# Kernel optimization log

Measured on AMD Instinct MI355X. Metric: run time of the kernel, lower is better.

## Reference

```python
import jax, jax.numpy as jnp
import numpy as np

B, S, D, H, L, V, DF = 2, 1024, 1024, 16, 4, 32000, 4096


def setup_inputs() -> dict:
    key = jax.random.key(0)
    ks = iter(jax.random.split(key, 64))
    rn = lambda shape, s=0.02: jax.random.normal(next(ks), shape, jnp.float32) * s
    inp = {
        'dec_input': rn((B, S, D), 1.0),
        'enc_input': rn((B, S, D), 1.0),
        # additive masks: causal for self-attn, none for cross-attn
        'masked_attention_mask': jnp.where(jnp.tril(jnp.ones((S, S), bool)), 0.0, -1e9)[None, None].astype(jnp.float32),
        'cross_attention_mask': jnp.zeros((1, 1, S, S), jnp.float32),
        'num_heads': H,
    }
    for p in ['sWq', 'sWk', 'sWv', 'sWo', 'cWq', 'cWk', 'cWv', 'cWo']:
        inp[p] = rn((L, D, D))
    for p in ['sbq', 'sbk', 'sbv', 'sbo', 'cbq', 'cbk', 'cbv', 'cbo']:
        inp[p] = jnp.zeros((L, D), jnp.float32)
    for p in ['ln1_g', 'ln2_g', 'ln3_g']:
        inp[p] = jnp.ones((L, D), jnp.float32)
    for p in ['ln1_b', 'ln2_b', 'ln3_b']:
        inp[p] = jnp.zeros((L, D), jnp.float32)
    inp['fW1'] = rn((L, D, DF)); inp['fb1'] = jnp.zeros((L, DF), jnp.float32)
    inp['fW2'] = rn((L, DF, D)); inp['fb2'] = jnp.zeros((L, D), jnp.float32)
    inp['Wout'] = rn((D, V)); inp['bout'] = jnp.zeros((V,), jnp.float32)
    return inp


def positional_encoding(seq_len, d_model, n=10000.0):
    # vectorized equivalent of the original triple-nested loop:
    # even d -> sin(i / n^(d/D)); odd d -> cos(i / n^((d-1)/D)); d==0 denom 1 == n^0
    i = jnp.arange(seq_len, dtype=jnp.float32)[:, None]
    d = jnp.arange(d_model)
    denom = jnp.power(n, (2 * (d // 2)).astype(jnp.float32) / d_model)
    ang = i / denom
    return jnp.where(d % 2 == 0, jnp.sin(ang), jnp.cos(ang))  # [S, D]


def layer_norm(x, g, b, eps=1e-5):
    m = jnp.mean(x, -1, keepdims=True)
    v = jnp.mean(jnp.square(x - m), -1, keepdims=True)
    return (x - m) * jax.lax.rsqrt(v + eps) * g + b


def mha(q_in, k_in, v_in, mask, Wq, bq, Wk, bk, Wv, bv, Wo, bo, h):
    b, sq, d = q_in.shape
    dh = d // h
    q = (q_in @ Wq + bq).reshape(b, sq, h, dh)
    k = (k_in @ Wk + bk).reshape(b, -1, h, dh)
    v = (v_in @ Wv + bv).reshape(b, -1, h, dh)
    scores = jnp.einsum('bqhd,bkhd->bhqk', q, k) / jnp.sqrt(jnp.float32(dh)) + mask
    attn = jax.nn.softmax(scores, axis=-1)
    out = jnp.einsum('bhqk,bkhd->bqhd', attn, v).reshape(b, sq, d)
    return out @ Wo + bo


def reference(dec_input, enc_input, masked_attention_mask, cross_attention_mask,
              sWq, sbq, sWk, sbk, sWv, sbv, sWo, sbo,
              cWq, cbq, cWk, cbk, cWv, cbv, cWo, cbo,
              ln1_g, ln1_b, ln2_g, ln2_b, ln3_g, ln3_b,
              fW1, fb1, fW2, fb2, Wout, bout, num_heads):
    b, s, d = dec_input.shape
    x0 = dec_input + positional_encoding(s, d)
    n_layers = sWq.shape[0]
    y = x0
    for l in range(n_layers):
        # NOTE: original DecoderSequential bug: every block consumes the ORIGINAL input;
        # only the last block's output survives.
        a1 = layer_norm(x0 + mha(x0, x0, x0, masked_attention_mask,
                                 sWq[l], sbq[l], sWk[l], sbk[l], sWv[l], sbv[l], sWo[l], sbo[l], num_heads),
                        ln1_g[l], ln1_b[l])
        a2 = layer_norm(a1 + mha(a1, enc_input, enc_input, cross_attention_mask,
                                 cWq[l], cbq[l], cWk[l], cbk[l], cWv[l], cbv[l], cWo[l], cbo[l], num_heads),
                        ln2_g[l], ln2_b[l])
        ff = jax.nn.relu(a2 @ fW1[l] + fb1[l]) @ fW2[l] + fb2[l]
        y = layer_norm(a2 + ff, ln3_g[l], ln3_b[l])
    return y @ Wout + bout  # [B, S, V]
```

## Files before the change

kernel.cpp:

```cpp
#include <hip/hip_runtime.h>
#include <cstdint>
#include <cstddef>

#define DEV __device__ __forceinline__

typedef __attribute__((ext_vector_type(8))) short short8;
typedef __attribute__((ext_vector_type(4))) float f32x4;
typedef __attribute__((ext_vector_type(16))) float f32x16;
typedef __attribute__((ext_vector_type(4))) unsigned short ushort4v;

DEV unsigned short f2bf(float f){
  union { float f; unsigned int i; } v; v.f = f;
  unsigned int r = v.i + 0x7fffu + ((v.i >> 16) & 1u);
  return (unsigned short)(r >> 16);
}

DEV void gld_lds16(const unsigned short* g, unsigned short* lds){
  __builtin_amdgcn_global_load_lds((const __attribute__((address_space(1))) void*)g,
                                   (__attribute__((address_space(3))) void*)lds, 16, 0, 0);
}

DEV int swz(int r, int s){
  int ln = r >> 1;
  int sl = ((r & 1) << 2) | s;
  return ln * 64 + (((sl ^ (ln & 7))) << 3);
}

template<int BN, int EPI>
__global__ __launch_bounds__(256, 2)
void gemm32(const unsigned short* __restrict__ A,
            const unsigned short* __restrict__ Bt,
            const float* __restrict__ bias,
            void* __restrict__ C, int M, int N, int K)
{
  constexpr int NFR  = BN / 64;
  constexpr int ROWS = 128 + BN;
  constexpr int BUFH = ROWS * 32;
  constexpr int GLD  = ROWS / 64;
  __shared__ __align__(16) unsigned short lds[3 * BUFH];

  const int tid = threadIdx.x, wid = tid >> 6, l = tid & 63;
  const int wr = wid >> 1, wcn = wid & 1;

  const int nbm = M / 128, nbn = N / BN;
  const int nwg = nbm * nbn;
  const int q8 = nwg >> 3, r8 = nwg & 7;
  const int xcd = blockIdx.x & 7, within = blockIdx.x >> 3;
  const int wg = (xcd < r8 ? xcd * (q8 + 1) : r8 * (q8 + 1) + (xcd - r8) * q8) + within;
  const int mb = (wg % nbm) * 128, nb = (wg / nbm) * BN;

  const int nk = K / 32;

  const int sL   = tid >> 3;
  const int sSl  = (tid & 7) ^ (sL & 7);
  const int sRow = sL * 2 + (sSl >> 2);
  const int sKc  = (sSl & 3) * 8;

  const int r31 = l & 31, hi = l >> 5;

  int aoff[2][2], boff[NFR][2];
  #pragma unroll
  for (int m = 0; m < 2; m++)
    #pragma unroll
    for (int ks = 0; ks < 2; ks++)
      aoff[m][ks] = wr * 2048 + swz(m * 32 + r31, 2 * ks + hi);
  #pragma unroll
  for (int n = 0; n < NFR; n++){
    const int col = wcn * (BN / 2) + n * 32 + r31;
    #pragma unroll
    for (int ks = 0; ks < 2; ks++)
      boff[n][ks] = 4096 + (col >> 6) * 2048 + swz(col & 63, 2 * ks + hi);
  }

  f32x16 acc[2][NFR];
  #pragma unroll
  for (int m = 0; m < 2; m++)
    #pragma unroll
    for (int n = 0; n < NFR; n++)
      #pragma unroll
      for (int e = 0; e < 16; e++) acc[m][n][e] = 0.f;

#define STAGE_A(c, tt, b2) \
  gld_lds16(A + (size_t)(mb + (c)*64 + sRow) * K + (size_t)(tt)*32 + sKc, \
            lds + (b2)*BUFH + (c)*2048 + tid*8)
#define STAGE_B(c, tt, b2) \
  gld_lds16(Bt + (size_t)(nb + (c)*64 + sRow) * K + (size_t)(tt)*32 + sKc, \
            lds + (b2)*BUFH + 4096 + (c)*2048 + tid*8)
#define WAIT_GLD() do { if constexpr (GLD == 6) asm volatile("s_waitcnt vmcnt(6)" ::: "memory"); \
                        else if constexpr (GLD == 4) asm volatile("s_waitcnt vmcnt(4)" ::: "memory"); \
                        else asm volatile("s_waitcnt vmcnt(3)" ::: "memory"); } while(0)

  STAGE_A(0, 0, 0); STAGE_A(1, 0, 0);
  #pragma unroll
  for (int c = 0; c < NFR; c++) STAGE_B(c, 0, 0);
  if (nk > 1){
    STAGE_A(0, 1, 1); STAGE_A(1, 1, 1);
    #pragma unroll
    for (int c = 0; c < NFR; c++) STAGE_B(c, 1, 1);
    WAIT_GLD();
  } else {
    asm volatile("s_waitcnt vmcnt(0)" ::: "memory");
  }
  asm volatile("" ::: "memory");
  __builtin_amdgcn_s_barrier();
  asm volatile("" ::: "memory");

  int bb = 0;
  for (int u = 0; u < nk; u++){
    const unsigned short* buf = lds + bb * BUFH;
    const int sb = (bb >= 1) ? bb - 1 : 2;
    const bool st = (u + 2 < nk);
    short8 af[2], bf[NFR];

    af[0] = *(const short8*)(buf + aoff[0][0]);
    af[1] = *(const short8*)(buf + aoff[1][0]);
    #pragma unroll
    for (int n = 0; n < NFR; n++) bf[n] = *(const short8*)(buf + boff[n][0]);
    if (st){
      STAGE_A(0, u + 2, sb); STAGE_A(1, u + 2, sb);
      if constexpr (NFR == 4) STAGE_B(0, u + 2, sb);
    }
    __builtin_amdgcn_s_setprio(1);
    #pragma unroll
    for (int m = 0; m < 2; m++)
      #pragma unroll
      for (int n = 0; n < NFR; n++)
        acc[m][n] = __builtin_amdgcn_mfma_f32_32x32x16_bf16(af[m], bf[n], acc[m][n], 0, 0, 0);
    __builtin_amdgcn_s_setprio(0);

    af[0] = *(const short8*)(buf + aoff[0][1]);
    af[1] = *(const short8*)(buf + aoff[1][1]);
    #pragma unroll
    for (int n = 0; n < NFR; n++) bf[n] = *(const short8*)(buf + boff[n][1]);
    if (st){
      if constexpr (NFR == 4){ STAGE_B(1, u + 2, sb); STAGE_B(2, u + 2, sb); STAGE_B(3, u + 2, sb); }
      else if constexpr (NFR == 2){ STAGE_B(0, u + 2, sb); STAGE_B(1, u + 2, sb); }
      else { STAGE_B(0, u + 2, sb); }
    }
    __builtin_amdgcn_s_setprio(1);
    #pragma unroll
    for (int m = 0; m < 2; m++)
      #pragma unroll
      for (int n = 0; n < NFR; n++)
        acc[m][n] = __builtin_amdgcn_mfma_f32_32x32x16_bf16(af[m], bf[n], acc[m][n], 0, 0, 0);
    __builtin_amdgcn_s_setprio(0);

    if (st)               WAIT_GLD();
    else if (u + 1 < nk)  asm volatile("s_waitcnt vmcnt(0)" ::: "memory");
    asm volatile("" ::: "memory");
    __builtin_amdgcn_s_barrier();
    asm volatile("" ::: "memory");
    bb = (bb == 2) ? 0 : bb + 1;
  }
#undef WAIT_GLD
#undef STAGE_A
#undef STAGE_B

  #pragma unroll
  for (int n = 0; n < NFR; n++){
    const int col = nb + wcn * (BN / 2) + n * 32 + r31;
    const float bv = bias ? bias[col] : 0.f;
    #pragma unroll
    for (int m = 0; m < 2; m++){
      const int rowb = mb + wr * 64 + m * 32 + 4 * hi;
      #pragma unroll
      for (int reg = 0; reg < 16; reg++){
        const int row = rowb + (reg & 3) + 8 * (reg >> 2);
        float v = acc[m][n][reg] + bv;
        size_t idx = (size_t)row * N + col;
        if (EPI == 0)       ((float*)C)[idx] = v;
        else if (EPI == 3)  __builtin_nontemporal_store(v, &((float*)C)[idx]);
        else if (EPI == 1)  ((unsigned short*)C)[idx] = f2bf(v);
        else { v = v > 0.f ? v : 0.f; ((unsigned short*)C)[idx] = f2bf(v); }
      }
    }
  }
}

template<int CAUSAL>
__global__ __launch_bounds__(256)
void attn_kernel(const unsigned short* __restrict__ Qb, int ldq,
                 const unsigned short* __restrict__ Kb, int ldk,
                 const unsigned short* __restrict__ Vb, int ldv,
                 unsigned short* __restrict__ Ob, int ldo)
{
  constexpr int S = 1024;
  __shared__ __align__(16) unsigned short vt[64][40];
  __shared__ __align__(16) unsigned short plds[4][16][40];
  const int tid = threadIdx.x, w = tid >> 6, l = tid & 63;
  const int qt = blockIdx.x, bh = blockIdx.y;
  const int b = bh >> 4, h = bh & 15;
  const int hoff = h * 64;
  const size_t rb = (size_t)b * S;

  const int qrow = qt * 64 + w * 16 + (l & 15);
  const unsigned short* qp = Qb + (rb + qrow) * ldq + hoff + ((l >> 4) * 8);
  short8 qf0 = *(const short8*)qp;
  short8 qf1 = *(const short8*)(qp + 32);

  float m_run[4] = {-1e30f, -1e30f, -1e30f, -1e30f};
  float l_run[4] = {0.f, 0.f, 0.f, 0.f};
  f32x4 oacc[4];
  #pragma unroll
  for (int t = 0; t < 4; t++) oacc[t] = (f32x4){0.f, 0.f, 0.f, 0.f};

  const int qmax = qt * 64 + w * 16 + 15;
  const int nkeys = CAUSAL ? (qt * 64 + 64) : S;
  const int skey = tid >> 3, sd8 = (tid & 7) * 8;

  for (int kb = 0; kb < nkeys; kb += 32){
    short8 vv = *(const short8*)(Vb + (rb + kb + skey) * ldv + hoff + sd8);
    #pragma unroll
    for (int i = 0; i < 8; i++) vt[sd8 + i][skey] = (unsigned short)vv[i];
    __syncthreads();
    if (!CAUSAL || kb <= qmax){
      f32x4 sc[2];
      #pragma unroll
      for (int g = 0; g < 2; g++){
        const unsigned short* kp = Kb + (rb + kb + g * 16 + (l & 15)) * ldk + hoff + ((l >> 4) * 8);
        short8 kf0 = *(const short8*)kp;
        short8 kf1 = *(const short8*)(kp + 32);
        f32x4 z = (f32x4){0.f, 0.f, 0.f, 0.f};
        z = __builtin_amdgcn_mfma_f32_16x16x32_bf16(qf0, kf0, z, 0, 0, 0);
        z = __builtin_amdgcn_mfma_f32_16x16x32_bf16(qf1, kf1, z, 0, 0, 0);
        sc[g] = z;
      }
      #pragma unroll
      for (int jj = 0; jj < 4; jj++){
        float s0 = sc[0][jj] * 0.125f, s1 = sc[1][jj] * 0.125f;
        if (CAUSAL){
          int q = qt * 64 + w * 16 + ((l >> 4) << 2) + jj;
          if (kb + (l & 15) > q)      s0 = -1e30f;
          if (kb + 16 + (l & 15) > q) s1 = -1e30f;
        }
        float mx = fmaxf(s0, s1);
        mx = fmaxf(mx, __shfl_xor(mx, 1));
        mx = fmaxf(mx, __shfl_xor(mx, 2));
        mx = fmaxf(mx, __shfl_xor(mx, 4));
        mx = fmaxf(mx, __shfl_xor(mx, 8));
        float mnew = fmaxf(m_run[jj], mx);
        float scal = __expf(m_run[jj] - mnew);
        m_run[jj] = mnew;
        float p0 = __expf(s0 - mnew), p1 = __expf(s1 - mnew);
        float rs = p0 + p1;
        rs += __shfl_xor(rs, 1); rs += __shfl_xor(rs, 2);
        rs += __shfl_xor(rs, 4); rs += __shfl_xor(rs, 8);
        l_run[jj] = l_run[jj] * scal + rs;
        #pragma unroll
        for (int t = 0; t < 4; t++) oacc[t][jj] *= scal;
        int qr = ((l >> 4) << 2) + jj;
        plds[w][qr][l & 15]      = f2bf(p0);
        plds[w][qr][16 + (l & 15)] = f2bf(p1);
      }
      asm volatile("s_waitcnt lgkmcnt(0)" ::: "memory");
      short8 pf = *(const short8*)&plds[w][l & 15][(l >> 4) * 8];
      #pragma unroll
      for (int t = 0; t < 4; t++){
        short8 vf = *(const short8*)&vt[t * 16 + (l & 15)][(l >> 4) * 8];
        oacc[t] = __builtin_amdgcn_mfma_f32_16x16x32_bf16(pf, vf, oacc[t], 0, 0, 0);
      }
    }
    __syncthreads();
  }
  #pragma unroll
  for (int jj = 0; jj < 4; jj++){
    float inv = 1.f / l_run[jj];
    int q = qt * 64 + w * 16 + ((l >> 4) << 2) + jj;
    #pragma unroll
    for (int t = 0; t < 4; t++)
      Ob[(rb + q) * ldo + hoff + t * 16 + (l & 15)] = f2bf(oacc[t][jj] * inv);
  }
}

__global__ __launch_bounds__(256)
void ln_kernel(const float* __restrict__ x1, const float* __restrict__ x2,
               const float* __restrict__ g, const float* __restrict__ be,
               float* __restrict__ outf, unsigned short* __restrict__ outb)
{
  const int row = blockIdx.x, t = threadIdx.x;
  __shared__ float red[4];
  const float4 v1 = ((const float4*)(x1 + (size_t)row * 1024))[t];
  const float4 v2 = ((const float4*)(x2 + (size_t)row * 1024))[t];
  float x[4] = {v1.x + v2.x, v1.y + v2.y, v1.z + v2.z, v1.w + v2.w};
  float s = x[0] + x[1] + x[2] + x[3];
  for (int o = 1; o < 64; o <<= 1) s += __shfl_xor(s, o);
  const int w = t >> 6, l = t & 63;
  if (l == 0) red[w] = s;
  __syncthreads();
  const float mean = (red[0] + red[1] + red[2] + red[3]) * (1.f / 1024.f);
  float d[4]; float sq = 0.f;
  #pragma unroll
  for (int i = 0; i < 4; i++){ d[i] = x[i] - mean; sq += d[i] * d[i]; }
  __syncthreads();
  for (int o = 1; o < 64; o <<= 1) sq += __shfl_xor(sq, o);
  if (l == 0) red[w] = sq;
  __syncthreads();
  const float var = (red[0] + red[1] + red[2] + red[3]) * (1.f / 1024.f);
  const float inv = rsqrtf(var + 1e-5f);
  const int base = t * 4;
  #pragma unroll
  for (int i = 0; i < 4; i++){
    float o = d[i] * inv * g[base + i] + be[base + i];
    if (outf) outf[(size_t)row * 1024 + base + i] = o;
    outb[(size_t)row * 1024 + base + i] = f2bf(o);
  }
}

__global__ __launch_bounds__(256)
void build_x0(const float* __restrict__ dec, float* __restrict__ xf, unsigned short* __restrict__ xb)
{
  const int i = blockIdx.x * 256 + threadIdx.x;
  const int i4 = i * 4;
  const int d0 = i4 & 1023;
  const int s  = (i4 >> 10) & 1023;
  float4 dv = ((const float4*)dec)[i];
  const float* dvp = (const float*)&dv;
  float o[4];
  #pragma unroll
  for (int j = 0; j < 4; j++){
    int dd = d0 + j;
    float e = (float)(dd & ~1) * (1.f / 1024.f);
    float den = expf(e * 9.210340371976184f);
    float ang = (float)s / den;
    float pe = (dd & 1) ? cosf(ang) : sinf(ang);
    o[j] = dvp[j] + pe;
  }
  ((float4*)xf)[i] = make_float4(o[0], o[1], o[2], o[3]);
  ushort4v ob; ob[0] = f2bf(o[0]); ob[1] = f2bf(o[1]); ob[2] = f2bf(o[2]); ob[3] = f2bf(o[3]);
  ((ushort4v*)xb)[i] = ob;
}

__global__ __launch_bounds__(256)
void cvt_bf16_k(const float* __restrict__ in, unsigned short* __restrict__ out)
{
  const int i = blockIdx.x * 256 + threadIdx.x;
  float4 v = ((const float4*)in)[i];
  ushort4v o; o[0] = f2bf(v.x); o[1] = f2bf(v.y); o[2] = f2bf(v.z); o[3] = f2bf(v.w);
  ((ushort4v*)out)[i] = o;
}

__global__ __launch_bounds__(256)
void transpose_cvt(const float* __restrict__ in, unsigned short* __restrict__ out, int R, int C)
{
  __shared__ float t[32][65];
  const int cb = blockIdx.x * 32, rb = blockIdx.y * 64;
  const int tx = threadIdx.x & 31, ty = threadIdx.x >> 5;
  #pragma unroll
  for (int i = 0; i < 8; i++)
    t[tx][ty + 8 * i] = in[(size_t)(rb + ty + 8 * i) * C + cb + tx];
  __syncthreads();
  const int lane = threadIdx.x & 63, cr = threadIdx.x >> 6;
  #pragma unroll
  for (int j = 0; j < 8; j++){
    int c = cr + 4 * j;
    out[(size_t)(cb + c) * R + rb + lane] = f2bf(t[c][lane]);
  }
}

struct TPtrs { const float* src[8]; unsigned short* dst[8]; };
__global__ __launch_bounds__(256)
void transpose_cvt8(TPtrs p)
{
  __shared__ float t[32][65];
  const float* __restrict__ in = p.src[blockIdx.z];
  unsigned short* __restrict__ out = p.dst[blockIdx.z];
  const int cb = blockIdx.x * 32, rb = blockIdx.y * 64;
  const int tx = threadIdx.x & 31, ty = threadIdx.x >> 5;
  #pragma unroll
  for (int i = 0; i < 8; i++)
    t[tx][ty + 8 * i] = in[(size_t)(rb + ty + 8 * i) * 1024 + cb + tx];
  __syncthreads();
  const int lane = threadIdx.x & 63, cr = threadIdx.x >> 6;
  #pragma unroll
  for (int j = 0; j < 8; j++){
    int c = cr + 4 * j;
    out[(size_t)(cb + c) * 1024 + rb + lane] = f2bf(t[c][lane]);
  }
}

__global__ __launch_bounds__(256)
void copy_biases(const float* sbq, const float* sbk, const float* sbv,
                 const float* cbk, const float* cbv,
                 float* bqkv, float* bkvc)
{
  const int i = blockIdx.x * 256 + threadIdx.x;
  const int seg = i >> 10, off = i & 1023;
  if (seg == 0)      bqkv[off] = sbq[off];
  else if (seg == 1) bqkv[1024 + off] = sbk[off];
  else if (seg == 2) bqkv[2048 + off] = sbv[off];
  else if (seg == 3) bkvc[off] = cbk[off];
  else               bkvc[1024 + off] = cbv[off];
}

extern "C" void kernel_launch(void* const* d_in, const int* in_sizes, int n_in,
                              void* d_out, int out_size, void* d_ws, size_t ws_size,
                              hipStream_t stream)
{
  constexpr int S = 1024, D = 1024, V = 32000, DF = 4096;
  constexpr int M = 2 * S;
  constexpr int DD = D * D;
  constexpr int l3 = 3;

  const float* dec  = (const float*)d_in[0];
  const float* enc  = (const float*)d_in[1];
  const float* sWq = (const float*)d_in[5]  + l3 * DD;
  const float* sWk = (const float*)d_in[6]  + l3 * DD;
  const float* sWv = (const float*)d_in[7]  + l3 * DD;
  const float* sWo = (const float*)d_in[8]  + l3 * DD;
  const float* cWq = (const float*)d_in[9]  + l3 * DD;
  const float* cWk = (const float*)d_in[10] + l3 * DD;
  const float* cWv = (const float*)d_in[11] + l3 * DD;
  const float* cWo = (const float*)d_in[12] + l3 * DD;
  const float* sbq = (const float*)d_in[13] + l3 * D;
  const float* sbk = (const float*)d_in[14] + l3 * D;
  const float* sbv = (const float*)d_in[15] + l3 * D;
  const float* sbo = (const float*)d_in[16] + l3 * D;
  const float* cbq = (const float*)d_in[17] + l3 * D;
  const float* cbk = (const float*)d_in[18] + l3 * D;
  const float* cbv = (const float*)d_in[19] + l3 * D;
  const float* cbo = (const float*)d_in[20] + l3 * D;
  const float* ln1g = (const float*)d_in[21] + l3 * D;
  const float* ln2g = (const float*)d_in[22] + l3 * D;
  const float* ln3g = (const float*)d_in[23] + l3 * D;
  const float* ln1b = (const float*)d_in[24] + l3 * D;
  const float* ln2b = (const float*)d_in[25] + l3 * D;
  const float* ln3b = (const float*)d_in[26] + l3 * D;
  const float* fW1 = (const float*)d_in[27] + (size_t)l3 * D * DF;
  const float* fb1 = (const float*)d_in[28] + l3 * DF;
  const float* fW2 = (const float*)d_in[29] + (size_t)l3 * DF * D;
  const float* fb2 = (const float*)d_in[30] + l3 * D;
  const float* Wout = (const float*)d_in[31];
  const float* bout = (const float*)d_in[32];
  float* out = (float*)d_out;

  uint8_t* wsp = (uint8_t*)d_ws;
  auto alloc = [&](size_t bytes) -> void* {
    void* p = wsp; wsp += (bytes + 255) & ~(size_t)255; return p;
  };
  float*          x0f  = (float*)alloc((size_t)M * D * 4);
  unsigned short* x0b  = (unsigned short*)alloc((size_t)M * D * 2);
  unsigned short* encb = (unsigned short*)alloc((size_t)M * D * 2);
  unsigned short* wqkv = (unsigned short*)alloc((size_t)3 * DD * 2);
  unsigned short* wos  = (unsigned short*)alloc((size_t)DD * 2);
  unsigned short* wqc  = (unsigned short*)alloc((size_t)DD * 2);
  unsigned short* wkvc = (unsigned short*)alloc((size_t)2 * DD * 2);
  unsigned short* woc  = (unsigned short*)alloc((size_t)DD * 2);
  unsigned short* wf1  = (unsigned short*)alloc((size_t)D * DF * 2);
  unsigned short* wf2  = (unsigned short*)alloc((size_t)D * DF * 2);
  unsigned short* wvo  = (unsigned short*)alloc((size_t)V * D * 2);
  float*          bqkv = (float*)alloc(3 * D * 4);
  float*          bkvc = (float*)alloc(2 * D * 4);
  unsigned short* qkv  = (unsigned short*)alloc((size_t)M * 3 * D * 2);
  unsigned short* attnb= (unsigned short*)alloc((size_t)M * D * 2);
  float*          oproj= (float*)alloc((size_t)M * D * 4);
  float*          a1f  = (float*)alloc((size_t)M * D * 4);
  unsigned short* a1b  = (unsigned short*)alloc((size_t)M * D * 2);
  unsigned short* qc   = (unsigned short*)alloc((size_t)M * D * 2);
  unsigned short* kvc  = (unsigned short*)alloc((size_t)M * 2 * D * 2);
  float*          a2f  = (float*)alloc((size_t)M * D * 4);
  unsigned short* a2b  = (unsigned short*)alloc((size_t)M * D * 2);
  unsigned short* ffh  = (unsigned short*)alloc((size_t)M * DF * 2);
  unsigned short* yb   = (unsigned short*)alloc((size_t)M * D * 2);

  build_x0<<<M * D / 4 / 256, 256, 0, stream>>>(dec, x0f, x0b);
  cvt_bf16_k<<<M * D / 4 / 256, 256, 0, stream>>>(enc, encb);

  TPtrs tp;
  tp.src[0] = sWq; tp.dst[0] = wqkv;
  tp.src[1] = sWk; tp.dst[1] = wqkv + DD;
  tp.src[2] = sWv; tp.dst[2] = wqkv + 2 * DD;
  tp.src[3] = sWo; tp.dst[3] = wos;
  tp.src[4] = cWq; tp.dst[4] = wqc;
  tp.src[5] = cWk; tp.dst[5] = wkvc;
  tp.src[6] = cWv; tp.dst[6] = wkvc + DD;
  tp.src[7] = cWo; tp.dst[7] = woc;
  transpose_cvt8<<<dim3(32, 16, 8), 256, 0, stream>>>(tp);
  transpose_cvt<<<dim3(DF/32, D/64), 256, 0, stream>>>(fW1, wf1, D, DF);
  transpose_cvt<<<dim3(D/32, DF/64), 256, 0, stream>>>(fW2, wf2, DF, D);
  transpose_cvt<<<dim3(V/32, D/64), 256, 0, stream>>>(Wout, wvo, D, V);
  copy_biases<<<20, 256, 0, stream>>>(sbq, sbk, sbv, cbk, cbv, bqkv, bkvc);

  gemm32<128,1><<<(M/128)*(3*D/128), 256, 0, stream>>>(x0b, wqkv, bqkv, qkv, M, 3*D, D);
  attn_kernel<1><<<dim3(S/64, 32), 256, 0, stream>>>(qkv, 3*D, qkv + D, 3*D, qkv + 2*D, 3*D, attnb, D);
  gemm32<64,0><<<(M/128)*(D/64), 256, 0, stream>>>(attnb, wos, sbo, oproj, M, D, D);
  ln_kernel<<<M, 256, 0, stream>>>(x0f, oproj, ln1g, ln1b, a1f, a1b);

  gemm32<64,1><<<(M/128)*(D/64), 256, 0, stream>>>(a1b, wqc, cbq, qc, M, D, D);
  gemm32<128,1><<<(M/128)*(2*D/128), 256, 0, stream>>>(encb, wkvc, bkvc, kvc, M, 2*D, D);
  attn_kernel<0><<<dim3(S/64, 32), 256, 0, stream>>>(qc, D, kvc, 2*D, kvc + D, 2*D, attnb, D);
  gemm32<64,0><<<(M/128)*(D/64), 256, 0, stream>>>(attnb, woc, cbo, oproj, M, D, D);
  ln_kernel<<<M, 256, 0, stream>>>(a1f, oproj, ln2g, ln2b, a2f, a2b);

  gemm32<256,2><<<(M/128)*(DF/256), 256, 0, stream>>>(a2b, wf1, fb1, ffh, M, DF, D);
  gemm32<64,0><<<(M/128)*(D/64), 256, 0, stream>>>(ffh, wf2, fb2, oproj, M, D, DF);
  ln_kernel<<<M, 256, 0, stream>>>(a2f, oproj, ln3g, ln3b, nullptr, yb);

  gemm32<256,3><<<(M/128)*(V/256), 256, 0, stream>>>(yb, wvo, bout, out, M, V, D);
}
```

Before: 603.6 us.

## Double-buffer K/V tiles in LDS with 64-key blocks in attention kernel

Rewrites the flash-attention inner loop to process 64 keys per iteration instead of 32. K tiles are staged into double-buffered LDS via global_load_lds with XOR swizzling, replacing per-wave direct global K loads. The next V tile is prefetched into registers and transposed into a swizzled LDS buffer while the current tile is being computed. The causal mask is applied only on the diagonal tile. The aim is to hide global memory latency, cut K reloads across waves, and halve the barrier count. In exchange it uses more LDS and registers, which could lower occupancy.

```diff
diff --git a/kernel.cpp b/kernel.cpp
--- a/kernel.cpp
+++ b/kernel.cpp
@@ -185,8 +185,10 @@
                  unsigned short* __restrict__ Ob, int ldo)
 {
   constexpr int S = 1024;
-  __shared__ __align__(16) unsigned short vt[64][40];
-  __shared__ __align__(16) unsigned short plds[4][16][40];
+  __shared__ __align__(16) unsigned short klds[2][4096];
+  __shared__ __align__(16) unsigned short vlds[2][4096];
+  __shared__ __align__(16) unsigned short plds[4][16][72];
+
   const int tid = threadIdx.x, w = tid >> 6, l = tid & 63;
   const int qt = blockIdx.x, bh = blockIdx.y;
   const int b = bh >> 4, h = bh & 15;
@@ -204,64 +206,126 @@
   #pragma unroll
   for (int t = 0; t < 4; t++) oacc[t] = (f32x4){0.f, 0.f, 0.f, 0.f};
 
-  const int qmax = qt * 64 + w * 16 + 15;
-  const int nkeys = CAUSAL ? (qt * 64 + 64) : S;
-  const int skey = tid >> 3, sd8 = (tid & 7) * 8;
-
-  for (int kb = 0; kb < nkeys; kb += 32){
-    short8 vv = *(const short8*)(Vb + (rb + kb + skey) * ldv + hoff + sd8);
-    #pragma unroll
-    for (int i = 0; i < 8; i++) vt[sd8 + i][skey] = (unsigned short)vv[i];
+  const int nkv = CAUSAL ? (qt + 1) : (S / 64);
+
+  const int sRowK  = tid >> 3;
+  const int sSlotK = (tid & 7) ^ ((tid >> 3) & 7);
+  const int skey   = tid >> 3;
+  const int sd8    = (tid & 7) * 8;
+
+  int koff[4][2];
+  #pragma unroll
+  for (int g = 0; g < 4; g++)
+    #pragma unroll
+    for (int hh = 0; hh < 2; hh++)
+      koff[g][hh] = (16 * g + (l & 15)) * 64 + (((hh * 4 + (l >> 4)) ^ (l & 7)) << 3);
+
+  const int vpar = (l >> 3) & 1;
+  int voff[4][2];
+  #pragma unroll
+  for (int t = 0; t < 4; t++)
+    #pragma unroll
+    for (int ks = 0; ks < 2; ks++)
+      voff[t][ks] = (16 * t + (l & 15)) * 64 +
+                    ((((ks * 4 + (l >> 4)) ^ (l & 7) ^ ((2 * t + vpar) & 7))) << 3);
+
+#define STAGE_K(c, kt, bf) \
+  gld_lds16(Kb + (rb + (size_t)(kt) * 64 + (c) * 32 + sRowK) * ldk + hoff + sSlotK * 8, \
+            &klds[bf][(c) * 2048 + tid * 8])
+#define LOAD_V(kt, r0v, r1v) do { \
+  r0v = *(const short8*)(Vb + (rb + (size_t)(kt) * 64 + skey) * ldv + hoff + sd8); \
+  r1v = *(const short8*)(Vb + (rb + (size_t)(kt) * 64 + 32 + skey) * ldv + hoff + sd8); } while(0)
+#define WRITE_VT(bf, p, vv) do { \
+  _Pragma("unroll") \
+  for (int i = 0; i < 8; i++){ \
+    vlds[bf][(sd8 + i) * 64 + (((w + 4 * (p)) ^ i ^ (l & 7)) << 3) + (l >> 3)] = \
+      (unsigned short)(vv)[i]; \
+  } } while(0)
+
+  short8 v0, v1;
+  STAGE_K(0, 0, 0); STAGE_K(1, 0, 0);
+  LOAD_V(0, v0, v1);
+  asm volatile("s_waitcnt vmcnt(0)" ::: "memory");
+  WRITE_VT(0, 0, v0); WRITE_VT(0, 1, v1);
+  __syncthreads();
+
+  for (int u = 0; u < nkv; u++){
+    const int cur = u & 1, nxt = cur ^ 1;
+    const bool pre = (u + 1 < nkv);
+    if (pre){ STAGE_K(0, u + 1, nxt); STAGE_K(1, u + 1, nxt); LOAD_V(u + 1, v0, v1); }
+
+    f32x4 sc[4];
+    #pragma unroll
+    for (int g = 0; g < 4; g++){
+      short8 k0 = *(const short8*)&klds[cur][koff[g][0]];
+      short8 k1 = *(const short8*)&klds[cur][koff[g][1]];
+      f32x4 z = (f32x4){0.f, 0.f, 0.f, 0.f};
+      z = __builtin_amdgcn_mfma_f32_16x16x32_bf16(qf0, k0, z, 0, 0, 0);
+      z = __builtin_amdgcn_mfma_f32_16x16x32_bf16(qf1, k1, z, 0, 0, 0);
+      sc[g] = z;
+    }
+
+    const bool diag = CAUSAL && (u == qt);
+    const int kb = u * 64;
+    #pragma unroll
+    for (int jj = 0; jj < 4; jj++){
+      float s0 = sc[0][jj] * 0.125f, s1 = sc[1][jj] * 0.125f;
+      float s2 = sc[2][jj] * 0.125f, s3 = sc[3][jj] * 0.125f;
+      if (diag){
+        const int q = qt * 64 + w * 16 + ((l >> 4) << 2) + jj;
+        const int ky = kb + (l & 15);
+        if (ky      > q) s0 = -1e30f;
+        if (ky + 16 > q) s1 = -1e30f;
+        if (ky + 32 > q) s2 = -1e30f;
+        if (ky + 48 > q) s3 = -1e30f;
+      }
+      float mx = fmaxf(fmaxf(s0, s1), fmaxf(s2, s3));
+      mx = fmaxf(mx, __shfl_xor(mx, 1));
+      mx = fmaxf(mx, __shfl_xor(mx, 2));
+      mx = fmaxf(mx, __shfl_xor(mx, 4));
+      mx = fmaxf(mx, __shfl_xor(mx, 8));
+      float mnew = fmaxf(m_run[jj], mx);
+      float scal = __expf(m_run[jj] - mnew);
+      m_run[jj] = mnew;
+      float p0 = __expf(s0 - mnew), p1 = __expf(s1 - mnew);
+      float p2 = __expf(s2 - mnew), p3 = __expf(s3 - mnew);
+      float rs = (p0 + p1) + (p2 + p3);
+      rs += __shfl_xor(rs, 1); rs += __shfl_xor(rs, 2);
+      rs += __shfl_xor(rs, 4); rs += __shfl_xor(rs, 8);
+      l_run[jj] = l_run[jj] * scal + rs;
+      #pragma unroll
+      for (int t = 0; t < 4; t++) oacc[t][jj] *= scal;
+      const int qr = ((l >> 4) << 2) + jj;
+      plds[w][qr][l & 15]        = f2bf(p0);
+      plds[w][qr][16 + (l & 15)] = f2bf(p1);
+      plds[w][qr][32 + (l & 15)] = f2bf(p2);
+      plds[w][qr][48 + (l & 15)] = f2bf(p3);
+    }
+    asm volatile("s_waitcnt lgkmcnt(0)" ::: "memory");
+    __builtin_amdgcn_sched_barrier(0);
+
+    short8 pf0 = *(const short8*)&plds[w][l & 15][(l >> 4) * 8];
+    short8 pf1 = *(const short8*)&plds[w][l & 15][32 + (l >> 4) * 8];
+    #pragma unroll
+    for (int t = 0; t < 4; t++){
+      short8 va = *(const short8*)&vlds[cur][voff[t][0]];
+      short8 vb2 = *(const short8*)&vlds[cur][voff[t][1]];
+      f32x4 o = oacc[t];
+      o = __builtin_amdgcn_mfma_f32_16x16x32_bf16(pf0, va,  o, 0, 0, 0);
+      o = __builtin_amdgcn_mfma_f32_16x16x32_bf16(pf1, vb2, o, 0, 0, 0);
+      oacc[t] = o;
+    }
+
+    if (pre){
+      asm volatile("s_waitcnt vmcnt(0)" ::: "memory");
+      WRITE_VT(nxt, 0, v0); WRITE_VT(nxt, 1, v1);
+    }
     __syncthreads();
-    if (!CAUSAL || kb <= qmax){
-      f32x4 sc[2];
-      #pragma unroll
-      for (int g = 0; g < 2; g++){
-        const unsigned short* kp = Kb + (rb + kb + g * 16 + (l & 15)) * ldk + hoff + ((l >> 4) * 8);
-        short8 kf0 = *(const short8*)kp;
-        short8 kf1 = *(const short8*)(kp + 32);
-        f32x4 z = (f32x4){0.f, 0.f, 0.f, 0.f};
-        z = __builtin_amdgcn_mfma_f32_16x16x32_bf16(qf0, kf0, z, 0, 0, 0);
-        z = __builtin_amdgcn_mfma_f32_16x16x32_bf16(qf1, kf1, z, 0, 0, 0);
-        sc[g] = z;
-      }
-      #pragma unroll
-      for (int jj = 0; jj < 4; jj++){
-        float s0 = sc[0][jj] * 0.125f, s1 = sc[1][jj] * 0.125f;
-        if (CAUSAL){
-          int q = qt * 64 + w * 16 + ((l >> 4) << 2) + jj;
-          if (kb + (l & 15) > q)      s0 = -1e30f;
-          if (kb + 16 + (l & 15) > q) s1 = -1e30f;
-        }
-        float mx = fmaxf(s0, s1);
-        mx = fmaxf(mx, __shfl_xor(mx, 1));
-        mx = fmaxf(mx, __shfl_xor(mx, 2));
-        mx = fmaxf(mx, __shfl_xor(mx, 4));
-        mx = fmaxf(mx, __shfl_xor(mx, 8));
-        float mnew = fmaxf(m_run[jj], mx);
-        float scal = __expf(m_run[jj] - mnew);
-        m_run[jj] = mnew;
-        float p0 = __expf(s0 - mnew), p1 = __expf(s1 - mnew);
-        float rs = p0 + p1;
-        rs += __shfl_xor(rs, 1); rs += __shfl_xor(rs, 2);
-        rs += __shfl_xor(rs, 4); rs += __shfl_xor(rs, 8);
-        l_run[jj] = l_run[jj] * scal + rs;
-        #pragma unroll
-        for (int t = 0; t < 4; t++) oacc[t][jj] *= scal;
-        int qr = ((l >> 4) << 2) + jj;
-        plds[w][qr][l & 15]      = f2bf(p0);
-        plds[w][qr][16 + (l & 15)] = f2bf(p1);
-      }
-      asm volatile("s_waitcnt lgkmcnt(0)" ::: "memory");
-      short8 pf = *(const short8*)&plds[w][l & 15][(l >> 4) * 8];
-      #pragma unroll
-      for (int t = 0; t < 4; t++){
-        short8 vf = *(const short8*)&vt[t * 16 + (l & 15)][(l >> 4) * 8];
-        oacc[t] = __builtin_amdgcn_mfma_f32_16x16x32_bf16(pf, vf, oacc[t], 0, 0, 0);
-      }
-    }
-    __syncthreads();
-  }
+  }
+#undef WRITE_VT
+#undef LOAD_V
+#undef STAGE_K
+
   #pragma unroll
   for (int jj = 0; jj < 4; jj++){
     float inv = 1.f / l_run[jj];
```

Measured after the change: 524.9 us (median of 2 runs). 1.15x faster.
